# Optimization experiments

Hardware: AMD Instinct MI355X
Metric: run time of the kernel (lower is better)

The kernel has to match this reference:

```python
import jax, jax.numpy as jnp
import numpy as np

B, N, H, E = 64, 512, 32, 4
N_STEPS = 5
ANNO = 1


def setup_inputs() -> dict:
    key = jax.random.key(0)
    ks = jax.random.split(key, 20)
    sc_h = 1.0 / np.sqrt(H)
    sc_3h = 1.0 / np.sqrt(3 * H)
    sc_ha = 1.0 / np.sqrt(H + ANNO)
    inp = {
        "x": jax.random.normal(ks[0], (B, N, H), jnp.float32),
        "a": jax.random.uniform(ks[1], (B, N, ANNO), jnp.float32),
        "m": jax.random.uniform(ks[2], (B, N, 2 * N * E), jnp.float32),
        # fc_in / fc_out: hidden -> hidden*n_edge (torch Linear: W [out,in])
        "W_in": jax.random.normal(ks[3], (H * E, H), jnp.float32) * sc_h,
        "b_in": jax.random.normal(ks[4], (H * E,), jnp.float32) * sc_h,
        "W_out": jax.random.normal(ks[5], (H * E, H), jnp.float32) * sc_h,
        "b_out": jax.random.normal(ks[6], (H * E,), jnp.float32) * sc_h,
        # GRU-style gates: 3*hidden -> hidden
        "Wz": jax.random.normal(ks[7], (H, 3 * H), jnp.float32) * sc_3h,
        "bz": jax.random.normal(ks[8], (H,), jnp.float32) * sc_3h,
        "Wr": jax.random.normal(ks[9], (H, 3 * H), jnp.float32) * sc_3h,
        "br": jax.random.normal(ks[10], (H,), jnp.float32) * sc_3h,
        "Wt": jax.random.normal(ks[11], (H, 3 * H), jnp.float32) * sc_3h,
        "bt": jax.random.normal(ks[12], (H,), jnp.float32) * sc_3h,
        # output head (task_id not in {18,19}): fc1, fc2
        "W1": jax.random.normal(ks[13], (H, H + ANNO), jnp.float32) * sc_ha,
        "b1": jax.random.normal(ks[14], (H,), jnp.float32) * sc_ha,
        "W2": jax.random.normal(ks[15], (1, H), jnp.float32) * sc_h,
        "b2": jax.random.normal(ks[16], (1,), jnp.float32) * sc_h,
    }
    return inp


def _reorder(s):
    # [B, N, H*E] -> view(B,N,H,E) -> transpose(2,3) -> transpose(1,2) -> [B, E*N, H]
    return s.reshape(B, N, H, E).transpose(0, 3, 1, 2).reshape(B, E * N, H)


def reference(x, a, m, W_in, b_in, W_out, b_out, Wz, bz, Wr, br, Wt, bt, W1, b1, W2, b2):
    m_in = m[:, :, : N * E]   # [B, N, N*E]
    m_out = m[:, :, N * E :]  # [B, N, N*E]
    h = x
    for _ in range(N_STEPS):
        s_in = _reorder(h @ W_in.T + b_in)    # [B, E*N, H]
        s_out = _reorder(h @ W_out.T + b_out)  # [B, E*N, H]
        a_in = jnp.einsum("bnm,bmh->bnh", m_in, s_in)
        a_out = jnp.einsum("bnm,bmh->bnh", m_out, s_out)
        cat = jnp.concatenate([a_in, a_out, h], axis=-1)  # [B, N, 3H]
        z = jax.nn.sigmoid(cat @ Wz.T + bz)
        r = jax.nn.sigmoid(cat @ Wr.T + br)
        joint = jnp.concatenate([a_in, a_out, r * h], axis=-1)
        h_hat = jnp.tanh(joint @ Wt.T + bt)
        h = (1.0 - z) * h + z * h_hat
    out = jnp.tanh(jnp.concatenate([h, a], axis=-1) @ W1.T + b1)  # [B, N, H]
    out = (out @ W2.T + b2).sum(-1)  # [B, N]
    return out
```

## Files before the change

### kernel.cpp

```cpp
#include <hip/hip_runtime.h>
#include <hip/hip_fp16.h>
#include <math.h>

#define B_ 64
#define N_ 512
#define H_ 32
#define E_ 4
#define NSTEPS 5
#define KTOT 2048
#define KSPLIT 4
#define KCHUNK 512
#define ASLAB (B_*N_*H_)

typedef _Float16 half8 __attribute__((ext_vector_type(8)));
typedef float   f32x4 __attribute__((ext_vector_type(4)));

__global__ __launch_bounds__(256) void k_init_h(const float* __restrict__ x,
                                                float* __restrict__ h) {
    int i = blockIdx.x * blockDim.x + threadIdx.x;
    ((f32x4*)h)[i] = ((const f32x4*)x)[i];
}

__global__ __launch_bounds__(256) void k_s(const float* __restrict__ hstate,
                                           const float* __restrict__ W_in,
                                           const float* __restrict__ b_in,
                                           const float* __restrict__ W_out,
                                           const float* __restrict__ b_out,
                                           _Float16* __restrict__ sT_in_hi,
                                           _Float16* __restrict__ sT_in_lo,
                                           _Float16* __restrict__ sT_out_hi,
                                           _Float16* __restrict__ sT_out_lo) {
    int b  = blockIdx.x >> 3;
    int n0 = (blockIdx.x & 7) * 64;
    int lane = threadIdx.x & 63;
    int w = __builtin_amdgcn_readfirstlane((int)(threadIdx.x >> 6));
    int n = n0 + lane;

    const float* hrow = hstate + ((size_t)b * N_ + n) * H_;
    f32x4 hv[8];
#pragma unroll
    for (int c = 0; c < 8; c++) hv[c] = ((const f32x4*)hrow)[c];

#pragma unroll 4
    for (int o = 0; o < 32; o++) {
        int he = w * 32 + o;
        const f32x4* wr = (const f32x4*)(W_in + (size_t)he * H_);
        float acc = b_in[he];
#pragma unroll
        for (int c = 0; c < 8; c++) {
            f32x4 wv = wr[c];
            acc += hv[c][0]*wv[0] + hv[c][1]*wv[1] + hv[c][2]*wv[2] + hv[c][3]*wv[3];
        }
        int hh = he >> 2, e = he & 3;
        size_t idx = ((size_t)b * H_ + hh) * KTOT + e * N_ + n;
        _Float16 hi = (_Float16)acc;
        sT_in_hi[idx] = hi;
        sT_in_lo[idx] = (_Float16)(acc - (float)hi);
    }
#pragma unroll 4
    for (int o = 0; o < 32; o++) {
        int he = w * 32 + o;
        const f32x4* wr = (const f32x4*)(W_out + (size_t)he * H_);
        float acc = b_out[he];
#pragma unroll
        for (int c = 0; c < 8; c++) {
            f32x4 wv = wr[c];
            acc += hv[c][0]*wv[0] + hv[c][1]*wv[1] + hv[c][2]*wv[2] + hv[c][3]*wv[3];
        }
        int hh = he >> 2, e = he & 3;
        size_t idx = ((size_t)b * H_ + hh) * KTOT + e * N_ + n;
        _Float16 hi = (_Float16)acc;
        sT_out_hi[idx] = hi;
        sT_out_lo[idx] = (_Float16)(acc - (float)hi);
    }
}

__global__ __launch_bounds__(256) void k_einsum_s(const float* __restrict__ m,
                                                  const _Float16* __restrict__ sT_in_hi,
                                                  const _Float16* __restrict__ sT_in_lo,
                                                  const _Float16* __restrict__ sT_out_hi,
                                                  const _Float16* __restrict__ sT_out_lo,
                                                  float* __restrict__ apart) {
    int z     = blockIdx.z;
    int dir   = z >> 2;
    int split = z & 3;
    int b     = blockIdx.y;
    int n0    = blockIdx.x * 64;
    int tid   = threadIdx.x;
    int w     = tid >> 6;
    int lane  = tid & 63;
    int l15   = lane & 15;
    int quad  = lane >> 4;

    const _Float16* sHi = (dir ? sT_out_hi : sT_in_hi) + (size_t)b * H_ * KTOT;
    const _Float16* sLo = (dir ? sT_out_lo : sT_in_lo) + (size_t)b * H_ * KTOT;
    float* aout = apart + (size_t)z * ASLAB;

    int row = n0 + w * 16 + l15;
    const float* mrow = m + ((size_t)b * N_ + row) * (2 * KTOT)
                          + (size_t)dir * KTOT + split * KCHUNK;

    f32x4 acc0 = {0.f,0.f,0.f,0.f}, acc1 = {0.f,0.f,0.f,0.f};

#pragma unroll 2
    for (int ks = 0; ks < KCHUNK; ks += 32) {
        int ko  = ks + quad * 8;
        int kos = split * KCHUNK + ko;
        f32x4 a0 = *(const f32x4*)(mrow + ko);
        f32x4 a1 = *(const f32x4*)(mrow + ko + 4);
        half8 Bhi0 = *(const half8*)(sHi + (size_t)l15        * KTOT + kos);
        half8 Bhi1 = *(const half8*)(sHi + (size_t)(l15 + 16) * KTOT + kos);
        half8 Blo0 = *(const half8*)(sLo + (size_t)l15        * KTOT + kos);
        half8 Blo1 = *(const half8*)(sLo + (size_t)(l15 + 16) * KTOT + kos);

        half8 Ahi, Alo;
#pragma unroll
        for (int j = 0; j < 4; j++) {
            float v0 = a0[j], v1 = a1[j];
            _Float16 h0 = (_Float16)v0, h1 = (_Float16)v1;
            Ahi[j]     = h0;
            Ahi[j + 4] = h1;
            Alo[j]     = (_Float16)(v0 - (float)h0);
            Alo[j + 4] = (_Float16)(v1 - (float)h1);
        }
        acc0 = __builtin_amdgcn_mfma_f32_16x16x32_f16(Ahi, Bhi0, acc0, 0, 0, 0);
        acc1 = __builtin_amdgcn_mfma_f32_16x16x32_f16(Ahi, Bhi1, acc1, 0, 0, 0);
        acc0 = __builtin_amdgcn_mfma_f32_16x16x32_f16(Ahi, Blo0, acc0, 0, 0, 0);
        acc1 = __builtin_amdgcn_mfma_f32_16x16x32_f16(Ahi, Blo1, acc1, 0, 0, 0);
        acc0 = __builtin_amdgcn_mfma_f32_16x16x32_f16(Alo, Bhi0, acc0, 0, 0, 0);
        acc1 = __builtin_amdgcn_mfma_f32_16x16x32_f16(Alo, Bhi1, acc1, 0, 0, 0);
    }

#pragma unroll
    for (int r = 0; r < 4; r++) {
        size_t rr = (size_t)b * N_ + (n0 + w * 16 + quad * 4 + r);
        aout[rr * H_ + l15]      = acc0[r];
        aout[rr * H_ + 16 + l15] = acc1[r];
    }
}

__global__ __launch_bounds__(256) void k_gate(const float* __restrict__ apart,
                                              float* __restrict__ hstate,
                                              const float* __restrict__ Wz,
                                              const float* __restrict__ bz,
                                              const float* __restrict__ Wr,
                                              const float* __restrict__ br,
                                              const float* __restrict__ Wt,
                                              const float* __restrict__ bt) {
    __shared__ float cat[8][96];
    __shared__ float rh[8][32];
    int base = blockIdx.x * 8;
    int t = threadIdx.x;

    for (int idx = t; idx < 768; idx += 256) {
        int r = idx / 96, c = idx - r * 96;
        size_t row = (size_t)(base + r);
        float v;
        if (c < 32) {
            const float* p = apart + row * 32 + c;
            v = ((p[0] + p[ASLAB]) + p[2 * (size_t)ASLAB]) + p[3 * (size_t)ASLAB];
        } else if (c < 64) {
            const float* p = apart + 4 * (size_t)ASLAB + row * 32 + (c - 32);
            v = ((p[0] + p[ASLAB]) + p[2 * (size_t)ASLAB]) + p[3 * (size_t)ASLAB];
        } else {
            v = hstate[row * 32 + (c - 64)];
        }
        cat[r][c] = v;
    }
    __syncthreads();

    int r = t >> 5, i = t & 31;
    float az = bz[i], ar = br[i];
    const f32x4* wzr = (const f32x4*)(Wz + (size_t)i * 96);
    const f32x4* wrr = (const f32x4*)(Wr + (size_t)i * 96);
    const f32x4* crow = (const f32x4*)cat[r];
#pragma unroll
    for (int kc = 0; kc < 24; kc++) {
        f32x4 cv = crow[kc];
        f32x4 wz = wzr[kc];
        f32x4 wr = wrr[kc];
        az += cv[0]*wz[0] + cv[1]*wz[1] + cv[2]*wz[2] + cv[3]*wz[3];
        ar += cv[0]*wr[0] + cv[1]*wr[1] + cv[2]*wr[2] + cv[3]*wr[3];
    }
    float z  = 1.f / (1.f + __expf(-az));
    float rg = 1.f / (1.f + __expf(-ar));
    float hold = cat[r][64 + i];
    rh[r][i] = rg * hold;
    __syncthreads();

    float at = bt[i];
    const f32x4* wtr = (const f32x4*)(Wt + (size_t)i * 96);
#pragma unroll
    for (int kc = 0; kc < 16; kc++) {
        f32x4 cv = crow[kc];
        f32x4 wt = wtr[kc];
        at += cv[0]*wt[0] + cv[1]*wt[1] + cv[2]*wt[2] + cv[3]*wt[3];
    }
    const f32x4* rrow = (const f32x4*)rh[r];
#pragma unroll
    for (int kc = 0; kc < 8; kc++) {
        f32x4 cv = rrow[kc];
        f32x4 wt = wtr[16 + kc];
        at += cv[0]*wt[0] + cv[1]*wt[1] + cv[2]*wt[2] + cv[3]*wt[3];
    }
    float hh = tanhf(at);
    hstate[(size_t)(base + r) * 32 + i] = (1.f - z) * hold + z * hh;
}

__global__ __launch_bounds__(256) void k_final(const float* __restrict__ hstate,
                                               const float* __restrict__ a,
                                               const float* __restrict__ W1,
                                               const float* __restrict__ b1,
                                               const float* __restrict__ W2,
                                               const float* __restrict__ b2,
                                               float* __restrict__ out) {
    __shared__ float hl[8][32];
    __shared__ float as[8];
    int base = blockIdx.x * 8;
    int t = threadIdx.x;
    {
        int r = t >> 5, c = t & 31;
        hl[r][c] = hstate[(size_t)(base + r) * 32 + c];
        if (t < 8) as[t] = a[base + t];
    }
    __syncthreads();
    int r = t >> 5, j = t & 31;
    float acc = b1[j];
    const float* w1r = W1 + (size_t)j * 33;
#pragma unroll
    for (int i2 = 0; i2 < 32; i2++) acc += hl[r][i2] * w1r[i2];
    acc += as[r] * w1r[32];
    float o = tanhf(acc) * W2[j];
#pragma unroll
    for (int off = 16; off; off >>= 1) o += __shfl_xor(o, off, 32);
    if (j == 0) out[base + r] = o + b2[0];
}

extern "C" void kernel_launch(void* const* d_in, const int* in_sizes, int n_in,
                              void* d_out, int out_size, void* d_ws, size_t ws_size,
                              hipStream_t stream) {
    const float* x     = (const float*)d_in[0];
    const float* a     = (const float*)d_in[1];
    const float* m     = (const float*)d_in[2];
    const float* W_in  = (const float*)d_in[3];
    const float* b_in  = (const float*)d_in[4];
    const float* W_out = (const float*)d_in[5];
    const float* b_out = (const float*)d_in[6];
    const float* Wz    = (const float*)d_in[7];
    const float* bz    = (const float*)d_in[8];
    const float* Wr    = (const float*)d_in[9];
    const float* br    = (const float*)d_in[10];
    const float* Wt    = (const float*)d_in[11];
    const float* bt    = (const float*)d_in[12];
    const float* W1    = (const float*)d_in[13];
    const float* b1    = (const float*)d_in[14];
    const float* W2    = (const float*)d_in[15];
    const float* b2    = (const float*)d_in[16];
    float* out = (float*)d_out;

    char* ws = (char*)d_ws;
    float*    h         = (float*)(ws);
    float*    apart     = (float*)(ws + ((size_t)4  << 20));
    _Float16* sT_in_hi  = (_Float16*)(ws + ((size_t)36 << 20));
    _Float16* sT_in_lo  = (_Float16*)(ws + ((size_t)44 << 20));
    _Float16* sT_out_hi = (_Float16*)(ws + ((size_t)52 << 20));
    _Float16* sT_out_lo = (_Float16*)(ws + ((size_t)60 << 20));

    k_init_h<<<1024, 256, 0, stream>>>(x, h);
    for (int s = 0; s < NSTEPS; s++) {
        k_s<<<512, 256, 0, stream>>>(h, W_in, b_in, W_out, b_out,
                                     sT_in_hi, sT_in_lo, sT_out_hi, sT_out_lo);
        k_einsum_s<<<dim3(8, 64, 8), 256, 0, stream>>>(m, sT_in_hi, sT_in_lo,
                                                       sT_out_hi, sT_out_lo, apart);
        k_gate<<<4096, 256, 0, stream>>>(apart, h, Wz, bz, Wr, br, Wt, bt);
    }
    k_final<<<4096, 256, 0, stream>>>(h, a, W1, b1, W2, b2, out);
}
```

Before: 2.530 ms.

## Stage s operand in swizzled LDS and loop over all rows per K-split

The einsum kernel now has each block own one (split, batch, direction) K-chunk. It loads the hi/lo fp16 s-operand slice into shared memory once, with an XOR swizzle to avoid bank conflicts, then sweeps all 512 rows in 8 passes. Before, every row block re-read the s operand from global memory. The K-split doubles to 8, which doubles the partial-sum buffer and the reduction reads in the gate kernel, and the grid drops to 1024 blocks that each do more serial work.

```diff
diff --git a/kernel.cpp b/kernel.cpp
--- a/kernel.cpp
+++ b/kernel.cpp
@@ -8,8 +8,8 @@
 #define E_ 4
 #define NSTEPS 5
 #define KTOT 2048
-#define KSPLIT 4
-#define KCHUNK 512
+#define KSPLIT 8
+#define KCHUNK 256
 #define ASLAB (B_*N_*H_)
 
 typedef _Float16 half8 __attribute__((ext_vector_type(8)));
@@ -75,67 +75,86 @@
     }
 }
 
-__global__ __launch_bounds__(256) void k_einsum_s(const float* __restrict__ m,
+__global__ __launch_bounds__(256) void k_einsum_l(const float* __restrict__ m,
                                                   const _Float16* __restrict__ sT_in_hi,
                                                   const _Float16* __restrict__ sT_in_lo,
                                                   const _Float16* __restrict__ sT_out_hi,
                                                   const _Float16* __restrict__ sT_out_lo,
                                                   float* __restrict__ apart) {
-    int z     = blockIdx.z;
-    int dir   = z >> 2;
-    int split = z & 3;
+    int split = blockIdx.x;
     int b     = blockIdx.y;
-    int n0    = blockIdx.x * 64;
+    int dir   = blockIdx.z;
     int tid   = threadIdx.x;
     int w     = tid >> 6;
     int lane  = tid & 63;
     int l15   = lane & 15;
     int quad  = lane >> 4;
 
-    const _Float16* sHi = (dir ? sT_out_hi : sT_in_hi) + (size_t)b * H_ * KTOT;
-    const _Float16* sLo = (dir ? sT_out_lo : sT_in_lo) + (size_t)b * H_ * KTOT;
-    float* aout = apart + (size_t)z * ASLAB;
-
-    int row = n0 + w * 16 + l15;
-    const float* mrow = m + ((size_t)b * N_ + row) * (2 * KTOT)
-                          + (size_t)dir * KTOT + split * KCHUNK;
-
-    f32x4 acc0 = {0.f,0.f,0.f,0.f}, acc1 = {0.f,0.f,0.f,0.f};
+    __shared__ __align__(16) char smem[32768];
+
+    const _Float16* sHi = (dir ? sT_out_hi : sT_in_hi)
+                          + (size_t)b * H_ * KTOT + split * KCHUNK;
+    const _Float16* sLo = (dir ? sT_out_lo : sT_in_lo)
+                          + (size_t)b * H_ * KTOT + split * KCHUNK;
+
+    for (int i = tid; i < 2048; i += 256) {
+        int plane = i >> 10, row = (i >> 5) & 31, c16 = i & 31;
+        const _Float16* src = (plane ? sLo : sHi) + (size_t)row * KTOT + c16 * 8;
+        half8 v = *(const half8*)src;
+        int byte = plane * 16384 + row * 512 + ((c16 * 16) ^ ((row & 7) << 4));
+        *(half8*)(smem + byte) = v;
+    }
+    __syncthreads();
+
+    float* aout = apart + (size_t)(dir * KSPLIT + split) * ASLAB;
+    int swz0 = (l15 & 7) << 4;
 
 #pragma unroll 2
-    for (int ks = 0; ks < KCHUNK; ks += 32) {
-        int ko  = ks + quad * 8;
-        int kos = split * KCHUNK + ko;
-        f32x4 a0 = *(const f32x4*)(mrow + ko);
-        f32x4 a1 = *(const f32x4*)(mrow + ko + 4);
-        half8 Bhi0 = *(const half8*)(sHi + (size_t)l15        * KTOT + kos);
-        half8 Bhi1 = *(const half8*)(sHi + (size_t)(l15 + 16) * KTOT + kos);
-        half8 Blo0 = *(const half8*)(sLo + (size_t)l15        * KTOT + kos);
-        half8 Blo1 = *(const half8*)(sLo + (size_t)(l15 + 16) * KTOT + kos);
-
-        half8 Ahi, Alo;
-#pragma unroll
-        for (int j = 0; j < 4; j++) {
-            float v0 = a0[j], v1 = a1[j];
-            _Float16 h0 = (_Float16)v0, h1 = (_Float16)v1;
-            Ahi[j]     = h0;
-            Ahi[j + 4] = h1;
-            Alo[j]     = (_Float16)(v0 - (float)h0);
-            Alo[j + 4] = (_Float16)(v1 - (float)h1);
-        }
-        acc0 = __builtin_amdgcn_mfma_f32_16x16x32_f16(Ahi, Bhi0, acc0, 0, 0, 0);
-        acc1 = __builtin_amdgcn_mfma_f32_16x16x32_f16(Ahi, Bhi1, acc1, 0, 0, 0);
-        acc0 = __builtin_amdgcn_mfma_f32_16x16x32_f16(Ahi, Blo0, acc0, 0, 0, 0);
-        acc1 = __builtin_amdgcn_mfma_f32_16x16x32_f16(Ahi, Blo1, acc1, 0, 0, 0);
-        acc0 = __builtin_amdgcn_mfma_f32_16x16x32_f16(Alo, Bhi0, acc0, 0, 0, 0);
-        acc1 = __builtin_amdgcn_mfma_f32_16x16x32_f16(Alo, Bhi1, acc1, 0, 0, 0);
-    }
-
-#pragma unroll
-    for (int r = 0; r < 4; r++) {
-        size_t rr = (size_t)b * N_ + (n0 + w * 16 + quad * 4 + r);
-        aout[rr * H_ + l15]      = acc0[r];
-        aout[rr * H_ + 16 + l15] = acc1[r];
+    for (int pass = 0; pass < 8; pass++) {
+        int n0 = pass * 64;
+        const float* mrow = m + ((size_t)b * N_ + n0 + w * 16 + l15) * (2 * KTOT)
+                              + (size_t)dir * KTOT + split * KCHUNK;
+
+        f32x4 acc0 = {0.f,0.f,0.f,0.f}, acc1 = {0.f,0.f,0.f,0.f};
+
+#pragma unroll 2
+        for (int it = 0; it < 8; it++) {
+            int ko = it * 32 + quad * 8;
+            f32x4 a0 = *(const f32x4*)(mrow + ko);
+            f32x4 a1 = *(const f32x4*)(mrow + ko + 4);
+
+            int kb = it * 64 + quad * 16;
+            int o0 = l15 * 512        + (kb ^ swz0);
+            int o1 = (l15 + 16) * 512 + (kb ^ swz0);
+            half8 Bhi0 = *(const half8*)(smem + o0);
+            half8 Bhi1 = *(const half8*)(smem + o1);
+            half8 Blo0 = *(const half8*)(smem + 16384 + o0);
+            half8 Blo1 = *(const half8*)(smem + 16384 + o1);
+
+            half8 Ahi, Alo;
+#pragma unroll
+            for (int j = 0; j < 4; j++) {
+                float v0 = a0[j], v1 = a1[j];
+                _Float16 h0 = (_Float16)v0, h1 = (_Float16)v1;
+                Ahi[j]     = h0;
+                Ahi[j + 4] = h1;
+                Alo[j]     = (_Float16)(v0 - (float)h0);
+                Alo[j + 4] = (_Float16)(v1 - (float)h1);
+            }
+            acc0 = __builtin_amdgcn_mfma_f32_16x16x32_f16(Ahi, Bhi0, acc0, 0, 0, 0);
+            acc1 = __builtin_amdgcn_mfma_f32_16x16x32_f16(Ahi, Bhi1, acc1, 0, 0, 0);
+            acc0 = __builtin_amdgcn_mfma_f32_16x16x32_f16(Ahi, Blo0, acc0, 0, 0, 0);
+            acc1 = __builtin_amdgcn_mfma_f32_16x16x32_f16(Ahi, Blo1, acc1, 0, 0, 0);
+            acc0 = __builtin_amdgcn_mfma_f32_16x16x32_f16(Alo, Bhi0, acc0, 0, 0, 0);
+            acc1 = __builtin_amdgcn_mfma_f32_16x16x32_f16(Alo, Bhi1, acc1, 0, 0, 0);
+        }
+
+#pragma unroll
+        for (int r = 0; r < 4; r++) {
+            size_t rr = (size_t)b * N_ + (n0 + w * 16 + quad * 4 + r);
+            aout[rr * H_ + l15]      = acc0[r];
+            aout[rr * H_ + 16 + l15] = acc1[r];
+        }
     }
 }
 
@@ -156,12 +175,12 @@
         int r = idx / 96, c = idx - r * 96;
         size_t row = (size_t)(base + r);
         float v;
-        if (c < 32) {
-            const float* p = apart + row * 32 + c;
-            v = ((p[0] + p[ASLAB]) + p[2 * (size_t)ASLAB]) + p[3 * (size_t)ASLAB];
-        } else if (c < 64) {
-            const float* p = apart + 4 * (size_t)ASLAB + row * 32 + (c - 32);
-            v = ((p[0] + p[ASLAB]) + p[2 * (size_t)ASLAB]) + p[3 * (size_t)ASLAB];
+        if (c < 64) {
+            int d = c >> 5;
+            const float* p = apart + (size_t)d * KSPLIT * ASLAB + row * 32 + (c & 31);
+            v = p[0];
+#pragma unroll
+            for (int s2 = 1; s2 < KSPLIT; s2++) v += p[(size_t)s2 * ASLAB];
         } else {
             v = hstate[row * 32 + (c - 64)];
         }
@@ -261,17 +280,18 @@
     char* ws = (char*)d_ws;
     float*    h         = (float*)(ws);
     float*    apart     = (float*)(ws + ((size_t)4  << 20));
-    _Float16* sT_in_hi  = (_Float16*)(ws + ((size_t)36 << 20));
-    _Float16* sT_in_lo  = (_Float16*)(ws + ((size_t)44 << 20));
-    _Float16* sT_out_hi = (_Float16*)(ws + ((size_t)52 << 20));
-    _Float16* sT_out_lo = (_Float16*)(ws + ((size_t)60 << 20));
+    _Float16* sT_in_hi  = (_Float16*)(ws + ((size_t)68 << 20));
+    _Float16* sT_in_lo  = (_Float16*)(ws + ((size_t)76 << 20));
+    _Float16* sT_out_hi = (_Float16*)(ws + ((size_t)84 << 20));
+    _Float16* sT_out_lo = (_Float16*)(ws + ((size_t)92 << 20));
 
     k_init_h<<<1024, 256, 0, stream>>>(x, h);
     for (int s = 0; s < NSTEPS; s++) {
         k_s<<<512, 256, 0, stream>>>(h, W_in, b_in, W_out, b_out,
                                      sT_in_hi, sT_in_lo, sT_out_hi, sT_out_lo);
-        k_einsum_s<<<dim3(8, 64, 8), 256, 0, stream>>>(m, sT_in_hi, sT_in_lo,
-                                                       sT_out_hi, sT_out_lo, apart);
+        k_einsum_l<<<dim3(KSPLIT, 64, 2), 256, 0, stream>>>(m, sT_in_hi, sT_in_lo,
+                                                            sT_out_hi, sT_out_lo,
+                                                            apart);
         k_gate<<<4096, 256, 0, stream>>>(apart, h, Wz, bz, Wr, br, Wt, bt);
     }
     k_final<<<4096, 256, 0, stream>>>(h, a, W1, b1, W2, b2, out);
```

New measurement: 2.401 ms. -5.1%, faster.
